# Performance work log

Measured on AMD Instinct MI355X. Metric: run time of the kernel, lower is better.

Reference implementation:

```python
import jax, jax.numpy as jnp
import numpy as np

E, K, D_IN, D_OUT, D_HID = 16, 2, 1024, 1024, 2048

def setup_inputs() -> dict:
    key = jax.random.key(0)
    ks = jax.random.split(key, 6)
    s_in = 1.0 / np.sqrt(D_IN)
    s_hid = 1.0 / np.sqrt(D_HID)
    return {
        "x": jax.random.normal(ks[0], (4096, D_IN), dtype=jnp.float32),
        "gate_w": jax.random.uniform(ks[1], (E, D_IN), jnp.float32, -s_in, s_in),
        "w1": jax.random.uniform(ks[2], (E, D_HID, D_IN), jnp.float32, -s_in, s_in),
        "b1": jax.random.uniform(ks[3], (E, D_HID), jnp.float32, -s_in, s_in),
        "w2": jax.random.uniform(ks[4], (E, D_OUT, D_HID), jnp.float32, -s_hid, s_hid),
        "b2": jax.random.uniform(ks[5], (E, D_OUT), jnp.float32, -s_hid, s_hid),
    }

def reference(x, gate_w, w1, b1, w2, b2):
    # gate: [B, E]
    gate_scores = jnp.einsum('bi,ei->be', x, gate_w)
    topk_vals, topk_idxs = jax.lax.top_k(gate_scores, K)  # [B, K]
    topk_weights = jax.nn.softmax(topk_vals, axis=-1)     # [B, K]
    # dense all-expert MLP (faithful to reference): [B, E, D_OUT]
    h = jax.nn.relu(jnp.einsum('bi,ehi->beh', x, w1) + b1[None])
    expert_outputs = jnp.einsum('beh,eoh->beo', h, w2) + b2[None]
    # gather selected experts: [B, K, D_OUT]
    sel = jnp.take_along_axis(expert_outputs, topk_idxs[:, :, None], axis=1)
    return jnp.sum(sel * topk_weights[:, :, None], axis=1)
```

## Files before the change

### kernel.cpp

```cpp
#include <hip/hip_runtime.h>
#include <hip/hip_bf16.h>
#include <math.h>

#define B_TOK 4096
#define NE 16
#define DI 1024
#define DH 2048
#define DOUT 1024
#define NSLOT (B_TOK * 2)

typedef unsigned short u16;
typedef short bfrag __attribute__((ext_vector_type(8)));
typedef float f32x4 __attribute__((ext_vector_type(4)));
typedef u16 u16x8 __attribute__((ext_vector_type(8)));

__device__ __forceinline__ u16 f2bf(float f) {
    union { float f; unsigned u; } v; v.f = f;
    return (u16)((v.u + 0x7fffu + ((v.u >> 16) & 1u)) >> 16);
}

__device__ __forceinline__ void async16(const void* g, void* lds) {
    __builtin_amdgcn_global_load_lds(
        (const __attribute__((address_space(1))) void*)g,
        (__attribute__((address_space(3))) void*)lds,
        16, 0, 0);
}

__global__ void zero_init(float* __restrict__ out, int n4) {
    int i = blockIdx.x * blockDim.x + threadIdx.x;
    if (i < n4) ((float4*)out)[i] = make_float4(0.f, 0.f, 0.f, 0.f);
}

__global__ void convert_bf16(const float* __restrict__ src, u16* __restrict__ dst, int n8) {
    int i = blockIdx.x * blockDim.x + threadIdx.x;
    if (i >= n8) return;
    const float4* s4 = (const float4*)src;
    float4 a = s4[2 * i], b = s4[2 * i + 1];
    u16x8 r;
    r[0] = f2bf(a.x); r[1] = f2bf(a.y); r[2] = f2bf(a.z); r[3] = f2bf(a.w);
    r[4] = f2bf(b.x); r[5] = f2bf(b.y); r[6] = f2bf(b.z); r[7] = f2bf(b.w);
    ((u16x8*)dst)[i] = r;
}

__global__ __launch_bounds__(256) void gate_topk(
    const float* __restrict__ x, const float* __restrict__ gw,
    int* __restrict__ token_e, float* __restrict__ token_w)
{
    int wave = threadIdx.x >> 6, lane = threadIdx.x & 63;
    int t = blockIdx.x * 4 + wave;
    const float4* x4 = (const float4*)(x + (size_t)t * DI);
    const float4* g4 = (const float4*)gw;
    double acc[NE];
#pragma unroll
    for (int e = 0; e < NE; ++e) acc[e] = 0.0;
#pragma unroll
    for (int i = 0; i < 4; ++i) {
        float4 xv = x4[lane + i * 64];
#pragma unroll
        for (int e = 0; e < NE; ++e) {
            float4 gv = g4[e * 256 + lane + i * 64];
            acc[e] += (double)xv.x * gv.x + (double)xv.y * gv.y
                    + (double)xv.z * gv.z + (double)xv.w * gv.w;
        }
    }
#pragma unroll
    for (int e = 0; e < NE; ++e) {
        double v = acc[e];
        for (int off = 32; off; off >>= 1) v += __shfl_xor(v, off, 64);
        acc[e] = v;
    }
    if (lane == 0) {
        int e0 = 0; double v0 = acc[0];
#pragma unroll
        for (int e = 1; e < NE; ++e) if (acc[e] > v0) { v0 = acc[e]; e0 = e; }
        int e1 = -1; double v1 = -1e300;
#pragma unroll
        for (int e = 0; e < NE; ++e) if (e != e0 && acc[e] > v1) { v1 = acc[e]; e1 = e; }
        float d = expf((float)(v1 - v0));
        float w0 = 1.f / (1.f + d);
        float w1 = d * w0;
        token_e[2 * t] = e0; token_e[2 * t + 1] = e1;
        token_w[2 * t] = w0; token_w[2 * t + 1] = w1;
    }
}

__global__ __launch_bounds__(1024) void route(
    const int* __restrict__ token_e, const float* __restrict__ token_w,
    int* __restrict__ counts, int* __restrict__ offsets,
    int* __restrict__ slot_token, float* __restrict__ slot_wgt)
{
    __shared__ int lcnt[NE];
    __shared__ int lcur[NE];
    int tid = threadIdx.x;
    if (tid < NE) lcnt[tid] = 0;
    __syncthreads();
    for (int i = tid; i < NSLOT; i += 1024) atomicAdd(&lcnt[token_e[i]], 1);
    __syncthreads();
    if (tid == 0) {
        int s = 0;
        for (int e = 0; e < NE; ++e) {
            int c = lcnt[e];
            counts[e] = c; offsets[e] = s; lcur[e] = s; s += c;
        }
    }
    __syncthreads();
    for (int i = tid; i < NSLOT; i += 1024) {
        int e = token_e[i];
        int pos = atomicAdd(&lcur[e], 1);
        slot_token[pos] = i >> 1;
        slot_wgt[pos] = token_w[i];
    }
}

template <int PHASE>
__global__ __launch_bounds__(512, 2) void moe_gemm(
    const u16* __restrict__ Abuf,
    const u16* __restrict__ Bbuf,
    const float* __restrict__ bias,
    const int* __restrict__ counts, const int* __restrict__ offsets,
    const int* __restrict__ slot_token, const float* __restrict__ slot_wgt,
    u16* __restrict__ hb, float* __restrict__ out)
{
    constexpr int KDIM = (PHASE == 1) ? DI : DH;
    constexpr int NDIM = (PHASE == 1) ? DH : DOUT;
    constexpr int BM = 256;
    constexpr int BN = (PHASE == 1) ? 256 : 128;
    constexpr int BK = 64;
    constexpr int WTM = (PHASE == 1) ? 128 : 64;
    constexpr int WTN = 64;
    constexpr int MF = WTM / 16, NF = WTN / 16;
    constexpr int GA = BM / 8;
    constexpr int GB = BN / 8;
    constexpr int GPW = (GA + GB) / 8;
    constexpr int BUFU = (BM + BN) * BK;
    constexpr int NT = NDIM / BN;
    constexpr int MT = B_TOK / BM;
    constexpr int PER_XCD = (NE * NT * MT) / 8;

    const int id = blockIdx.x;
    const int wg = (id & 7) * PER_XCD + (id >> 3);
    const int e  = wg / (NT * MT);
    const int rem = wg % (NT * MT);
    const int nt = rem / MT;
    const int mt = rem % MT;

    const int cnt = counts[e];
    const int m0 = mt * BM;
    if (m0 >= cnt) return;
    const int n0 = nt * BN;
    const int sbase = offsets[e];

    __shared__ u16 lds[2][BUFU];

    const int tid = threadIdx.x;
    const int wv = tid >> 6, lane = tid & 63;
    const int quad = lane >> 4, mr = lane & 15;
    const int wr = (PHASE == 1) ? (wv >> 2) : (wv >> 1);
    const int wc = (PHASE == 1) ? (wv & 3)  : (wv & 1);

    const int sr_ = lane >> 3, sc_ = lane & 7;
    const int sw = (sc_ ^ sr_) * 8;
    const u16* gptr[GPW];
#pragma unroll
    for (int j = 0; j < GPW; ++j) {
        const int G = wv * GPW + j;
        if (G < GA) {
            int row = G * 8 + sr_;
            if (PHASE == 1) {
                int rr = m0 + row; if (rr > cnt - 1) rr = cnt - 1;
                gptr[j] = Abuf + (size_t)slot_token[sbase + rr] * KDIM + sw;
            } else {
                int sr2 = sbase + m0 + row; if (sr2 > NSLOT - 1) sr2 = NSLOT - 1;
                gptr[j] = Abuf + (size_t)sr2 * KDIM + sw;
            }
        } else {
            int row = (G - GA) * 8 + sr_;
            gptr[j] = Bbuf + (size_t)e * NDIM * KDIM + (size_t)(n0 + row) * KDIM + sw;
        }
    }

    f32x4 acc[MF][NF];
#pragma unroll
    for (int i = 0; i < MF; ++i)
#pragma unroll
        for (int j = 0; j < NF; ++j) acc[i][j] = (f32x4){0.f, 0.f, 0.f, 0.f};

    const int nk = KDIM / BK;

#pragma unroll
    for (int j = 0; j < GPW; ++j)
        async16(gptr[j], &lds[0][(wv * GPW + j) * 512]);
    __syncthreads();

    for (int kt = 0; kt < nk; ++kt) {
        const int bb = kt & 1;
        if (kt + 1 < nk) {
#pragma unroll
            for (int j = 0; j < GPW; ++j)
                async16(gptr[j] + (kt + 1) * BK, &lds[bb ^ 1][(wv * GPW + j) * 512]);
        }
        const u16* al = &lds[bb][0];
        const u16* bl = al + BM * BK;
#pragma unroll
        for (int ks = 0; ks < 2; ++ks) {
            const int cp = ((ks * 4 + quad) ^ (mr & 7)) * 8;
            bfrag bf[NF];
#pragma unroll
            for (int nf = 0; nf < NF; ++nf)
                bf[nf] = *(const bfrag*)(bl + (wc * WTN + nf * 16 + mr) * BK + cp);
#pragma unroll
            for (int mf = 0; mf < MF; ++mf) {
                bfrag af = *(const bfrag*)(al + (wr * WTM + mf * 16 + mr) * BK + cp);
#pragma unroll
                for (int nf = 0; nf < NF; ++nf)
                    acc[mf][nf] = __builtin_amdgcn_mfma_f32_16x16x32_bf16(af, bf[nf], acc[mf][nf], 0, 0, 0);
            }
        }
        __syncthreads();
    }

    const float* bias_e = bias + e * NDIM;
    if constexpr (PHASE == 1) {
#pragma unroll
        for (int mf = 0; mf < MF; ++mf) {
            int mbase = wr * WTM + mf * 16 + quad * 4;
#pragma unroll
            for (int nf = 0; nf < NF; ++nf) {
                int n = n0 + wc * WTN + nf * 16 + mr;
                float bv = bias_e[n];
#pragma unroll
                for (int r = 0; r < 4; ++r) {
                    int m = m0 + mbase + r;
                    if (m < cnt) {
                        float v = acc[mf][nf][r] + bv;
                        v = v > 0.f ? v : 0.f;
                        hb[(size_t)(sbase + m) * DH + n] = f2bf(v);
                    }
                }
            }
        }
    } else {
#pragma unroll
        for (int mf = 0; mf < MF; ++mf) {
            int mbase = wr * WTM + mf * 16 + quad * 4;
#pragma unroll
            for (int r = 0; r < 4; ++r) {
                int m = m0 + mbase + r;
                if (m < cnt) {
                    int slot = sbase + m;
                    int tok = slot_token[slot];
                    float wgt = slot_wgt[slot];
                    float* orow = out + (size_t)tok * DOUT + n0 + wc * WTN;
#pragma unroll
                    for (int nf = 0; nf < NF; ++nf) {
                        int nl = nf * 16 + mr;
                        float v = wgt * (acc[mf][nf][r] + bias_e[n0 + wc * WTN + nl]);
                        atomicAdd(orow + nl, v);
                    }
                }
            }
        }
    }
}

extern "C" void kernel_launch(void* const* d_in, const int* in_sizes, int n_in,
                              void* d_out, int out_size, void* d_ws, size_t ws_size,
                              hipStream_t stream) {
    const float* x  = (const float*)d_in[0];
    const float* gw = (const float*)d_in[1];
    const float* w1 = (const float*)d_in[2];
    const float* b1 = (const float*)d_in[3];
    const float* w2 = (const float*)d_in[4];
    const float* b2 = (const float*)d_in[5];
    float* out = (float*)d_out;

    char* ws = (char*)d_ws;
    u16* xb = (u16*)ws;
    u16* wb = (u16*)(ws + 8388608);
    u16* hb = (u16*)(ws + 8388608 + 67108864);
    char* rb = ws + 109051904;
    int*   counts     = (int*)(rb);
    int*   offsets    = (int*)(rb + 64);
    int*   token_e    = (int*)(rb + 192);
    float* token_w    = (float*)(rb + 192 + 32768);
    int*   slot_token = (int*)(rb + 192 + 65536);
    float* slot_wgt   = (float*)(rb + 192 + 98304);

    zero_init<<<4096, 256, 0, stream>>>(out, (B_TOK * DOUT) / 4);
    convert_bf16<<<2048, 256, 0, stream>>>(x, xb, (B_TOK * DI) / 8);
    convert_bf16<<<16384, 256, 0, stream>>>(w1, wb, (NE * DH * DI) / 8);
    gate_topk<<<1024, 256, 0, stream>>>(x, gw, token_e, token_w);
    route<<<1, 1024, 0, stream>>>(token_e, token_w, counts, offsets, slot_token, slot_wgt);
    moe_gemm<1><<<NE * (DH / 256) * (B_TOK / 256) * 16 / 16, 512, 0, stream>>>(
        xb, wb, b1, counts, offsets, slot_token, slot_wgt, hb, out);
    convert_bf16<<<16384, 256, 0, stream>>>(w2, wb, (NE * DOUT * DH) / 8);
    moe_gemm<2><<<NE * (DOUT / 128) * (B_TOK / 256), 512, 0, stream>>>(
        hb, wb, b2, counts, offsets, slot_token, slot_wgt, hb, out);
}
```

Baseline: 558.2 us.

## Use 128x128 single-buffered GEMM tiles, split-K phase 2, fuse x conversion into gate

```diff
diff --git a/kernel.cpp b/kernel.cpp
--- a/kernel.cpp
+++ b/kernel.cpp
@@ -12,6 +12,7 @@
 typedef unsigned short u16;
 typedef short bfrag __attribute__((ext_vector_type(8)));
 typedef float f32x4 __attribute__((ext_vector_type(4)));
+typedef u16 u16x4 __attribute__((ext_vector_type(4)));
 typedef u16 u16x8 __attribute__((ext_vector_type(8)));
 
 __device__ __forceinline__ u16 f2bf(float f) {
@@ -44,18 +45,22 @@
 
 __global__ __launch_bounds__(256) void gate_topk(
     const float* __restrict__ x, const float* __restrict__ gw,
-    int* __restrict__ token_e, float* __restrict__ token_w)
+    int* __restrict__ token_e, float* __restrict__ token_w,
+    u16* __restrict__ xb)
 {
     int wave = threadIdx.x >> 6, lane = threadIdx.x & 63;
     int t = blockIdx.x * 4 + wave;
     const float4* x4 = (const float4*)(x + (size_t)t * DI);
     const float4* g4 = (const float4*)gw;
+    u16x4* xb4 = (u16x4*)(xb + (size_t)t * DI);
     double acc[NE];
 #pragma unroll
     for (int e = 0; e < NE; ++e) acc[e] = 0.0;
 #pragma unroll
     for (int i = 0; i < 4; ++i) {
         float4 xv = x4[lane + i * 64];
+        u16x4 xc; xc[0] = f2bf(xv.x); xc[1] = f2bf(xv.y); xc[2] = f2bf(xv.z); xc[3] = f2bf(xv.w);
+        xb4[lane + i * 64] = xc;
 #pragma unroll
         for (int e = 0; e < NE; ++e) {
             float4 gv = g4[e * 256 + lane + i * 64];
@@ -113,7 +118,7 @@
 }
 
 template <int PHASE>
-__global__ __launch_bounds__(512, 2) void moe_gemm(
+__global__ __launch_bounds__(256, 4) void moe_gemm(
     const u16* __restrict__ Abuf,
     const u16* __restrict__ Bbuf,
     const float* __restrict__ bias,
@@ -121,42 +126,40 @@
     const int* __restrict__ slot_token, const float* __restrict__ slot_wgt,
     u16* __restrict__ hb, float* __restrict__ out)
 {
-    constexpr int KDIM = (PHASE == 1) ? DI : DH;
+    constexpr int KDIM_T = (PHASE == 1) ? DI : DH;
+    constexpr int KB = 1024;
+    constexpr int NS = (PHASE == 1) ? 1 : 2;
     constexpr int NDIM = (PHASE == 1) ? DH : DOUT;
-    constexpr int BM = 256;
-    constexpr int BN = (PHASE == 1) ? 256 : 128;
-    constexpr int BK = 64;
-    constexpr int WTM = (PHASE == 1) ? 128 : 64;
-    constexpr int WTN = 64;
-    constexpr int MF = WTM / 16, NF = WTN / 16;
-    constexpr int GA = BM / 8;
-    constexpr int GB = BN / 8;
-    constexpr int GPW = (GA + GB) / 8;
-    constexpr int BUFU = (BM + BN) * BK;
+    constexpr int BM = 128, BN = 128, BK = 64;
+    constexpr int GA = BM / 8, GB = BN / 8;
+    constexpr int GPW = (GA + GB) / 4;
     constexpr int NT = NDIM / BN;
     constexpr int MT = B_TOK / BM;
-    constexpr int PER_XCD = (NE * NT * MT) / 8;
+    constexpr int TOTAL = NE * NS * NT * MT;
+    constexpr int PER_XCD = TOTAL / 8;
 
     const int id = blockIdx.x;
     const int wg = (id & 7) * PER_XCD + (id >> 3);
-    const int e  = wg / (NT * MT);
-    const int rem = wg % (NT * MT);
-    const int nt = rem / MT;
-    const int mt = rem % MT;
+    const int e   = wg / (NS * NT * MT);
+    int rem = wg % (NS * NT * MT);
+    const int sp  = rem / (NT * MT);
+    rem %= (NT * MT);
+    const int nt  = rem / MT;
+    const int mt  = rem % MT;
 
     const int cnt = counts[e];
     const int m0 = mt * BM;
     if (m0 >= cnt) return;
     const int n0 = nt * BN;
     const int sbase = offsets[e];
-
-    __shared__ u16 lds[2][BUFU];
+    const int koff = sp * KB;
+
+    __shared__ u16 lds[(BM + BN) * BK];
 
     const int tid = threadIdx.x;
     const int wv = tid >> 6, lane = tid & 63;
     const int quad = lane >> 4, mr = lane & 15;
-    const int wr = (PHASE == 1) ? (wv >> 2) : (wv >> 1);
-    const int wc = (PHASE == 1) ? (wv & 3)  : (wv & 1);
+    const int wr = wv >> 1, wc = wv & 1;
 
     const int sr_ = lane >> 3, sc_ = lane & 7;
     const int sw = (sc_ ^ sr_) * 8;
@@ -168,51 +171,43 @@
             int row = G * 8 + sr_;
             if (PHASE == 1) {
                 int rr = m0 + row; if (rr > cnt - 1) rr = cnt - 1;
-                gptr[j] = Abuf + (size_t)slot_token[sbase + rr] * KDIM + sw;
+                gptr[j] = Abuf + (size_t)slot_token[sbase + rr] * KDIM_T + koff + sw;
             } else {
-                int sr2 = sbase + m0 + row; if (sr2 > NSLOT - 1) sr2 = NSLOT - 1;
-                gptr[j] = Abuf + (size_t)sr2 * KDIM + sw;
+                int s2 = sbase + m0 + row; if (s2 > NSLOT - 1) s2 = NSLOT - 1;
+                gptr[j] = Abuf + (size_t)s2 * KDIM_T + koff + sw;
             }
         } else {
             int row = (G - GA) * 8 + sr_;
-            gptr[j] = Bbuf + (size_t)e * NDIM * KDIM + (size_t)(n0 + row) * KDIM + sw;
-        }
-    }
-
-    f32x4 acc[MF][NF];
-#pragma unroll
-    for (int i = 0; i < MF; ++i)
-#pragma unroll
-        for (int j = 0; j < NF; ++j) acc[i][j] = (f32x4){0.f, 0.f, 0.f, 0.f};
-
-    const int nk = KDIM / BK;
-
-#pragma unroll
-    for (int j = 0; j < GPW; ++j)
-        async16(gptr[j], &lds[0][(wv * GPW + j) * 512]);
-    __syncthreads();
-
+            gptr[j] = Bbuf + (size_t)e * NDIM * KDIM_T + (size_t)(n0 + row) * KDIM_T + koff + sw;
+        }
+    }
+
+    f32x4 acc[4][4];
+#pragma unroll
+    for (int i = 0; i < 4; ++i)
+#pragma unroll
+        for (int j = 0; j < 4; ++j) acc[i][j] = (f32x4){0.f, 0.f, 0.f, 0.f};
+
+    constexpr int nk = KB / BK;
     for (int kt = 0; kt < nk; ++kt) {
-        const int bb = kt & 1;
-        if (kt + 1 < nk) {
-#pragma unroll
-            for (int j = 0; j < GPW; ++j)
-                async16(gptr[j] + (kt + 1) * BK, &lds[bb ^ 1][(wv * GPW + j) * 512]);
-        }
-        const u16* al = &lds[bb][0];
+#pragma unroll
+        for (int j = 0; j < GPW; ++j)
+            async16(gptr[j] + kt * BK, &lds[(wv * GPW + j) * 512]);
+        __syncthreads();
+        const u16* al = &lds[0];
         const u16* bl = al + BM * BK;
 #pragma unroll
         for (int ks = 0; ks < 2; ++ks) {
             const int cp = ((ks * 4 + quad) ^ (mr & 7)) * 8;
-            bfrag bf[NF];
-#pragma unroll
-            for (int nf = 0; nf < NF; ++nf)
-                bf[nf] = *(const bfrag*)(bl + (wc * WTN + nf * 16 + mr) * BK + cp);
-#pragma unroll
-            for (int mf = 0; mf < MF; ++mf) {
-                bfrag af = *(const bfrag*)(al + (wr * WTM + mf * 16 + mr) * BK + cp);
-#pragma unroll
-                for (int nf = 0; nf < NF; ++nf)
+            bfrag bf[4];
+#pragma unroll
+            for (int nf = 0; nf < 4; ++nf)
+                bf[nf] = *(const bfrag*)(bl + (wc * 64 + nf * 16 + mr) * BK + cp);
+#pragma unroll
+            for (int mf = 0; mf < 4; ++mf) {
+                bfrag af = *(const bfrag*)(al + (wr * 64 + mf * 16 + mr) * BK + cp);
+#pragma unroll
+                for (int nf = 0; nf < 4; ++nf)
                     acc[mf][nf] = __builtin_amdgcn_mfma_f32_16x16x32_bf16(af, bf[nf], acc[mf][nf], 0, 0, 0);
             }
         }
@@ -222,11 +217,11 @@
     const float* bias_e = bias + e * NDIM;
     if constexpr (PHASE == 1) {
 #pragma unroll
-        for (int mf = 0; mf < MF; ++mf) {
-            int mbase = wr * WTM + mf * 16 + quad * 4;
-#pragma unroll
-            for (int nf = 0; nf < NF; ++nf) {
-                int n = n0 + wc * WTN + nf * 16 + mr;
+        for (int mf = 0; mf < 4; ++mf) {
+            int mbase = wr * 64 + mf * 16 + quad * 4;
+#pragma unroll
+            for (int nf = 0; nf < 4; ++nf) {
+                int n = n0 + wc * 64 + nf * 16 + mr;
                 float bv = bias_e[n];
 #pragma unroll
                 for (int r = 0; r < 4; ++r) {
@@ -241,8 +236,8 @@
         }
     } else {
 #pragma unroll
-        for (int mf = 0; mf < MF; ++mf) {
-            int mbase = wr * WTM + mf * 16 + quad * 4;
+        for (int mf = 0; mf < 4; ++mf) {
+            int mbase = wr * 64 + mf * 16 + quad * 4;
 #pragma unroll
             for (int r = 0; r < 4; ++r) {
                 int m = m0 + mbase + r;
@@ -250,12 +245,13 @@
                     int slot = sbase + m;
                     int tok = slot_token[slot];
                     float wgt = slot_wgt[slot];
-                    float* orow = out + (size_t)tok * DOUT + n0 + wc * WTN;
-#pragma unroll
-                    for (int nf = 0; nf < NF; ++nf) {
+                    float* orow = out + (size_t)tok * DOUT + n0 + wc * 64;
+#pragma unroll
+                    for (int nf = 0; nf < 4; ++nf) {
                         int nl = nf * 16 + mr;
-                        float v = wgt * (acc[mf][nf][r] + bias_e[n0 + wc * WTN + nl]);
-                        atomicAdd(orow + nl, v);
+                        float v = acc[mf][nf][r];
+                        if (sp == 0) v += bias_e[n0 + wc * 64 + nl];
+                        atomicAdd(orow + nl, wgt * v);
                     }
                 }
             }
@@ -287,13 +283,12 @@
     float* slot_wgt   = (float*)(rb + 192 + 98304);
 
     zero_init<<<4096, 256, 0, stream>>>(out, (B_TOK * DOUT) / 4);
-    convert_bf16<<<2048, 256, 0, stream>>>(x, xb, (B_TOK * DI) / 8);
     convert_bf16<<<16384, 256, 0, stream>>>(w1, wb, (NE * DH * DI) / 8);
-    gate_topk<<<1024, 256, 0, stream>>>(x, gw, token_e, token_w);
+    gate_topk<<<1024, 256, 0, stream>>>(x, gw, token_e, token_w, xb);
     route<<<1, 1024, 0, stream>>>(token_e, token_w, counts, offsets, slot_token, slot_wgt);
-    moe_gemm<1><<<NE * (DH / 256) * (B_TOK / 256) * 16 / 16, 512, 0, stream>>>(
+    moe_gemm<1><<<NE * 1 * (DH / 128) * (B_TOK / 128), 256, 0, stream>>>(
         xb, wb, b1, counts, offsets, slot_token, slot_wgt, hb, out);
     convert_bf16<<<16384, 256, 0, stream>>>(w2, wb, (NE * DOUT * DH) / 8);
-    moe_gemm<2><<<NE * (DOUT / 128) * (B_TOK / 256), 512, 0, stream>>>(
+    moe_gemm<2><<<NE * 2 * (DOUT / 128) * (B_TOK / 128), 256, 0, stream>>>(
         hb, wb, b2, counts, offsets, slot_token, slot_wgt, hb, out);
 }
```

After: 494.0 us. 1.13x faster.
